# Performance work log

Hardware: AMD Instinct MI355X
Metric: run time of the kernel (lower is better)

Reference implementation:

```python
import jax, jax.numpy as jnp
import numpy as np

E, H, V, P, RAW = 512, 1024, 12000, 36, 2048
B, L = 128, 21

def setup_inputs() -> dict:
    key = jax.random.key(0)
    ks = jax.random.split(key, 16)
    n = lambda k, sh: (0.02 * jax.random.normal(k, sh)).astype(jnp.float32)
    z = lambda sh: jnp.zeros(sh, jnp.float32)
    return {
        "images_features": jax.random.normal(ks[0], (B, P, RAW), dtype=jnp.float32),
        "encoded_captions": jax.random.randint(ks[1], (B, L), 0, V),
        "caption_lengths": L,
        "W_img": n(ks[2], (RAW, H)), "b_img": z((H,)),
        "W_glob": n(ks[3], (H, E)), "b_glob": z((E,)),
        "W_ih1": n(ks[4], (2 * E + H, 4 * H)), "W_hh1": n(ks[5], (H, 4 * H)),
        "b_ih1": z((4 * H,)), "b_hh1": z((4 * H,)),
        "Wx_gate": n(ks[6], (2 * E + H, H)), "bx_gate": z((H,)),
        "Wh_gate": n(ks[7], (H, H)), "bh_gate": z((H,)),
        "W_ih2": n(ks[8], (2 * H, 4 * H)), "W_hh2": n(ks[9], (H, 4 * H)),
        "b_ih2": z((4 * H,)), "b_hh2": z((4 * H,)),
        "Wv": n(ks[10], (H, P)), "bv": z((P,)),
        "Ws": n(ks[11], (H, P)), "bs": z((P,)),
        "Wg": n(ks[12], (H, P)),
        "wh": n(ks[13], (P,)),
        "emb": n(ks[14], (V, E)),
        "W_fc": n(ks[15], (H, V)), "b_fc": z((V,)),
    }

def _lstm(x, h, c, W_ih, W_hh, b_ih, b_hh):
    # torch LSTMCell gate order: i, f, g, o
    g = x @ W_ih + b_ih + h @ W_hh + b_hh
    i, f, gg, o = jnp.split(g, 4, axis=-1)
    c_new = jax.nn.sigmoid(f) * c + jax.nn.sigmoid(i) * jnp.tanh(gg)
    h_new = jax.nn.sigmoid(o) * jnp.tanh(c_new)
    return h_new, c_new

def reference(images_features, encoded_captions, caption_lengths, W_img, b_img,
              W_glob, b_glob, W_ih1, W_hh1, b_ih1, b_hh1, Wx_gate, bx_gate,
              Wh_gate, bh_gate, W_ih2, W_hh2, b_ih2, b_hh2, Wv, bv, Ws, bs,
              Wg, wh, emb, W_fc, b_fc):
    Bsz = images_features.shape[0]
    Hd = W_hh1.shape[0]
    T = int(caption_lengths) - 1
    Vfeat = jax.nn.relu(images_features @ W_img + b_img)            # (B,P,H)
    glob = jax.nn.relu(jnp.mean(Vfeat, axis=1) @ W_glob + b_glob)   # (B,E)
    img_proj = Vfeat @ Wv + bv                                      # (B,P,P) loop-invariant
    word_embs = emb[encoded_captions[:, :T]]                        # (B,T,E)

    def step(carry, we):
        h1, c1, h2, c2 = carry
        xt = jnp.concatenate([h2, glob, we], axis=-1)               # (B, H+2E)
        h1n, c1n = _lstm(xt, h1, c1, W_ih1, W_hh1, b_ih1, b_hh1)
        sen_gate = jax.nn.sigmoid(xt @ Wx_gate + bx_gate + h1 @ Wh_gate + bh_gate)
        st = sen_gate * jnp.tanh(c1n)                               # visual sentinel
        ht_proj = h1n @ Wg                                          # (B,P)
        z = jnp.tanh(img_proj + ht_proj[:, :, None]) @ wh           # (B,P)
        alpha = jax.nn.softmax(z, axis=1)                           # (B,P)
        context = jnp.einsum('bp,bph->bh', alpha, Vfeat)            # (B,H)
        att_vs = jnp.tanh(st @ Ws + bs + ht_proj) @ wh              # (B,)
        alpha_hat = jax.nn.softmax(jnp.concatenate([z, att_vs[:, None]], axis=1), axis=1)
        beta = alpha_hat[:, -1:]                                    # (B,1)
        c_hat = beta * st + (1.0 - beta) * context
        h2n, c2n = _lstm(jnp.concatenate([c_hat, h1n], axis=-1), h2, c2,
                         W_ih2, W_hh2, b_ih2, b_hh2)
        score = (c_hat + h2n) @ W_fc + b_fc                         # (B,V)
        return (h1n, c1n, h2n, c2n), (score, alpha, beta)

    zeros = jnp.zeros((Bsz, Hd), images_features.dtype)
    init = (zeros, zeros, zeros, zeros)
    _, (preds, alphas, betas) = jax.lax.scan(step, init, jnp.swapaxes(word_embs, 0, 1))
    return (jnp.swapaxes(preds, 0, 1),   # (B,T,V)
            jnp.swapaxes(alphas, 0, 1),  # (B,T,P)
            jnp.swapaxes(betas, 0, 1))   # (B,T,1)
```

## Files before the change

### kernel.cpp

```cpp
#include <hip/hip_runtime.h>
#include <hip/hip_bf16.h>
#include <math.h>

typedef __attribute__((ext_vector_type(4))) float f32x4;
typedef __attribute__((ext_vector_type(8))) short bf16x8;

constexpr int kB = 128, kT = 20, kH = 1024, kE = 512, kP = 36, kRaw = 2048, kV = 12000;
constexpr int kSlab1 = kB * 5120;
constexpr int kSlab2 = kB * 4096;

__device__ __forceinline__ float sigf(float x) { return 1.0f / (1.0f + expf(-x)); }

#define AS1C const __attribute__((address_space(1))) void*
#define AS3P __attribute__((address_space(3))) void*

constexpr int NZ1 = 2 * kB * kH / 4;
constexpr int NZ2 = 2 * kB * kH * 2 / 16;
constexpr int NCV = kB * kP * kRaw / 4;
constexpr int NPV = 64 * 1024 * 2 / 16;
constexpr int NPF = 32 * 1024 * 2 / 16;
constexpr int NPB = 5120;
constexpr int NGE = kB * kT * kE;

__global__ __launch_bounds__(256) void prep_small(
    float* c1z, uint4* h1z, const float* images, __hip_bfloat16* imagesb,
    uint4* wtv, uint4* wtfc_pad,
    const float* b_ih1, const float* b_hh1, const float* bx, const float* bh,
    const float* b_ih2, const float* b_hh2, float* bias_g1, float* bias_g2,
    const int* caps, const float* emb, __hip_bfloat16* wembb) {
  long idx = (long)blockIdx.x * 256 + threadIdx.x;
  if (idx < NZ1) { reinterpret_cast<float4*>(c1z)[idx] = make_float4(0, 0, 0, 0); return; }
  idx -= NZ1;
  if (idx < NZ2) { h1z[idx] = make_uint4(0, 0, 0, 0); return; }
  idx -= NZ2;
  if (idx < NCV) {
    float4 v = reinterpret_cast<const float4*>(images)[idx];
    __hip_bfloat16* d = imagesb + idx * 4;
    d[0] = __float2bfloat16(v.x); d[1] = __float2bfloat16(v.y);
    d[2] = __float2bfloat16(v.z); d[3] = __float2bfloat16(v.w);
    return;
  }
  idx -= NCV;
  if (idx < NPV) { wtv[idx] = make_uint4(0, 0, 0, 0); return; }
  idx -= NPV;
  if (idx < NPF) { wtfc_pad[idx] = make_uint4(0, 0, 0, 0); return; }
  idx -= NPF;
  if (idx < NPB) {
    int i = (int)idx;
    if (i < 4096) {
      bias_g1[i] = b_ih1[i] + b_hh1[i];
      bias_g2[i] = b_ih2[i] + b_hh2[i];
    } else {
      bias_g1[i] = bx[i - 4096] + bh[i - 4096];
    }
    return;
  }
  idx -= NPB;
  if (idx < NGE) {
    int e = (int)(idx % kE);
    int bt = (int)(idx / kE);
    int t = bt % kT;
    int b = bt / kT;
    int tok = caps[b * (kT + 1) + t];
    wembb[idx] = __float2bfloat16(emb[(size_t)tok * kE + e]);
  }
}

struct TJob {
  const float* src; __hip_bfloat16* dst;
  int ld_src, K, N, lddst, koff, noff, blk_off, nbx;
};
struct TAll { TJob job[12]; int njobs; int total_blocks; };

__global__ __launch_bounds__(256) void transpose_all(TAll ta) {
  __shared__ float t[32][33];
  int bid = blockIdx.x;
  int ji = 0;
  while (ji + 1 < ta.njobs && bid >= ta.job[ji + 1].blk_off) ++ji;
  const TJob& J = ta.job[ji];
  int lbid = bid - J.blk_off;
  int n0 = (lbid % J.nbx) * 32, k0 = (lbid / J.nbx) * 32;
  int tx = threadIdx.x & 31, ty = threadIdx.x >> 5;
  #pragma unroll
  for (int i = 0; i < 32; i += 8) {
    int k = k0 + ty + i, n = n0 + tx;
    t[ty + i][tx] = (k < J.K && n < J.N) ? J.src[(size_t)k * J.ld_src + n] : 0.0f;
  }
  __syncthreads();
  #pragma unroll
  for (int i = 0; i < 32; i += 8) {
    int n = n0 + ty + i, k = k0 + tx;
    if (n < J.N && k < J.K)
      J.dst[(size_t)(n + J.noff) * J.lddst + k + J.koff] = __float2bfloat16(t[tx][ty + i]);
  }
}

struct SegB { const __hip_bfloat16* A; int lda; int kstart; int kend; };
struct GemmBArgs {
  SegB seg[4]; int nseg;
  const __hip_bfloat16* WT; int ldk;
  const float* bias;
  float* C; __hip_bfloat16* C16; int ldc; int N; int Ktot; int act; int zstride;
};

__global__ __launch_bounds__(256) void gemm_bf16(GemmBArgs ga) {
  __shared__ char lds[65536];
  const int bm = blockIdx.y * 64;
  const int bn = blockIdx.x * 64;
  const int tid = threadIdx.x;
  const int lane = tid & 63;
  const int w = tid >> 6;
  const int wr = w >> 1, wc = w & 1;

  int rowS[4], scbS[4], dstS[4];
  #pragma unroll
  for (int j = 0; j < 4; ++j) {
    int off = ((j * 4 + w) * 64 + lane) * 16;
    int row = off >> 8, colb = off & 255;
    rowS[j] = row;
    scbS[j] = colb ^ ((row & 7) << 4);
    dstS[j] = (j * 4 + w) * 1024;
  }

  f32x4 acc[2][2] = {};
  const int nz = gridDim.z;
  const int nit = (ga.Ktot >> 7) / nz;
  const int it0 = blockIdx.z * nit;
  float* C = ga.C + (size_t)blockIdx.z * ga.zstride;

  auto stage = [&](int it, int buf) {
    const int k0 = it << 7;
    int si = 0;
    while (k0 >= ga.seg[si].kend) ++si;
    const __hip_bfloat16* Aseg = ga.seg[si].A;
    const int lda = ga.seg[si].lda;
    const int ks = k0 - ga.seg[si].kstart;
    char* baseA = lds + buf * 32768;
    char* baseB = baseA + 16384;
    #pragma unroll
    for (int j = 0; j < 4; ++j) {
      const __hip_bfloat16* sA = Aseg + (size_t)(bm + rowS[j]) * lda + ks + (scbS[j] >> 1);
      __builtin_amdgcn_global_load_lds((AS1C)sA, (AS3P)(baseA + dstS[j]), 16, 0, 0);
      const __hip_bfloat16* sB = ga.WT + (size_t)(bn + rowS[j]) * ga.ldk + k0 + (scbS[j] >> 1);
      __builtin_amdgcn_global_load_lds((AS1C)sB, (AS3P)(baseB + dstS[j]), 16, 0, 0);
    }
  };

  auto compute = [&](int buf) {
    const char* baseA = lds + buf * 32768;
    const char* baseB = baseA + 16384;
    #pragma unroll
    for (int kk = 0; kk < 4; ++kk) {
      bf16x8 a[2], b[2];
      #pragma unroll
      for (int f = 0; f < 2; ++f) {
        int row = wr * 32 + f * 16 + (lane & 15);
        int cb = kk * 64 + (lane >> 4) * 16;
        a[f] = *(const bf16x8*)(baseA + row * 256 + (cb ^ ((row & 7) << 4)));
        int nl = wc * 32 + f * 16 + (lane & 15);
        b[f] = *(const bf16x8*)(baseB + nl * 256 + (cb ^ ((nl & 7) << 4)));
      }
      #pragma unroll
      for (int fm = 0; fm < 2; ++fm)
        #pragma unroll
        for (int fn = 0; fn < 2; ++fn)
          acc[fm][fn] = __builtin_amdgcn_mfma_f32_16x16x32_bf16(a[fm], b[fn], acc[fm][fn], 0, 0, 0);
    }
  };

  stage(it0, 0);
  stage(it0 + 1, 1);
  asm volatile("s_waitcnt vmcnt(8)" ::: "memory");
  __builtin_amdgcn_s_barrier();
  int cur = 0;
  for (int i = 0; i < nit; ++i) {
    compute(cur);
    __builtin_amdgcn_s_barrier();
    if (i + 2 < nit) stage(it0 + i + 2, cur);
    if (i + 1 < nit) {
      if (i + 2 < nit) asm volatile("s_waitcnt vmcnt(8)" ::: "memory");
      else             asm volatile("s_waitcnt vmcnt(0)" ::: "memory");
      __builtin_amdgcn_s_barrier();
    }
    cur ^= 1;
  }

  #pragma unroll
  for (int fm = 0; fm < 2; ++fm) {
    int rbase = bm + wr * 32 + fm * 16 + (lane >> 4) * 4;
    #pragma unroll
    for (int fn = 0; fn < 2; ++fn) {
      int col = bn + wc * 32 + fn * 16 + (lane & 15);
      if (col >= ga.N) continue;
      float bv = ga.bias ? ga.bias[col] : 0.0f;
      #pragma unroll
      for (int j = 0; j < 4; ++j) {
        float v = acc[fm][fn][j] + bv;
        if (ga.act == 1) v = fmaxf(v, 0.0f);
        size_t off = (size_t)(rbase + j) * ga.ldc + col;
        if (ga.C) C[off] = v;
        if (ga.C16) ga.C16[off] = __float2bfloat16(v);
      }
    }
  }
}

struct G128Args {
  const __hip_bfloat16* A; int lda;
  const __hip_bfloat16* WT; int ldk;
  const float* bias;
  float* C; __hip_bfloat16* C16; int ldc; int N; int Ktot; int act; int cmap; int morder;
};

template <int BK>
__global__ __launch_bounds__(256) void gemm128(G128Args ga) {
  constexpr int RB = BK * 2;
  constexpr int TILEB = 128 * RB;
  constexpr int ROUNDS = TILEB / 4096;
  constexpr int SWZ = (RB == 256) ? 15 : (RB == 128 ? 7 : 3);
  __shared__ char lds[2 * 2 * TILEB];
  const int gx = gridDim.x;
  const int gy = gridDim.y;
  const int nwg = gx * gy;
  int bid = blockIdx.y * gx + blockIdx.x;
  int q = nwg >> 3, r = nwg & 7;
  int xc = bid & 7, yq = bid >> 3;
  int swz = (xc < r ? xc * (q + 1) : r * (q + 1) + (xc - r) * q) + yq;
  int bn, bm;
  if (ga.morder == 1) { bm = (swz % gy) * 128; bn = (swz / gy) * 128; }
  else                { bn = (swz % gx) * 128; bm = (swz / gx) * 128; }

  const int tid = threadIdx.x;
  const int lane = tid & 63;
  const int w = tid >> 6;
  const int wr = w >> 1, wc = w & 1;

  int rowS[ROUNDS], scbS[ROUNDS], dstS[ROUNDS];
  #pragma unroll
  for (int j = 0; j < ROUNDS; ++j) {
    int off = ((j * 4 + w) * 64 + lane) * 16;
    int row = off / RB, colb = off % RB;
    rowS[j] = row;
    scbS[j] = colb ^ ((row & SWZ) << 4);
    dstS[j] = off;
  }

  f32x4 acc[4][4] = {};
  const int nit = ga.Ktot / BK;

  auto stage = [&](int it, int buf) {
    const int k0 = it * BK;
    char* baseA = lds + buf * 2 * TILEB;
    char* baseB = baseA + TILEB;
    #pragma unroll
    for (int j = 0; j < ROUNDS; ++j) {
      const __hip_bfloat16* sA = ga.A + (size_t)(bm + rowS[j]) * ga.lda + k0 + (scbS[j] >> 1);
      __builtin_amdgcn_global_load_lds((AS1C)sA, (AS3P)(baseA + dstS[j]), 16, 0, 0);
      const __hip_bfloat16* sB = ga.WT + (size_t)(bn + rowS[j]) * ga.ldk + k0 + (scbS[j] >> 1);
      __builtin_amdgcn_global_load_lds((AS1C)sB, (AS3P)(baseB + dstS[j]), 16, 0, 0);
    }
  };

  auto compute = [&](int buf) {
    const char* baseA = lds + buf * 2 * TILEB;
    const char* baseB = baseA + TILEB;
    #pragma unroll
    for (int kk = 0; kk < BK / 32; ++kk) {
      bf16x8 a[4], b[4];
      int cb = kk * 64 + (lane >> 4) * 16;
      #pragma unroll
      for (int f = 0; f < 4; ++f) {
        int row = wr * 64 + f * 16 + (lane & 15);
        a[f] = *(const bf16x8*)(baseA + row * RB + (cb ^ ((row & SWZ) << 4)));
        int nl = wc * 64 + f * 16 + (lane & 15);
        b[f] = *(const bf16x8*)(baseB + nl * RB + (cb ^ ((nl & SWZ) << 4)));
      }
      #pragma unroll
      for (int fm = 0; fm < 4; ++fm)
        #pragma unroll
        for (int fn = 0; fn < 4; ++fn)
          acc[fm][fn] = __builtin_amdgcn_mfma_f32_16x16x32_bf16(a[fm], b[fn], acc[fm][fn], 0, 0, 0);
    }
  };

  auto wait_one_stage = [&]() {
    if constexpr (ROUNDS == 4) asm volatile("s_waitcnt vmcnt(8)" ::: "memory");
    else                       asm volatile("s_waitcnt vmcnt(4)" ::: "memory");
  };

  stage(0, 0);
  stage(1, 1);
  wait_one_stage();
  __builtin_amdgcn_s_barrier();
  int cur = 0;
  for (int i = 0; i < nit; ++i) {
    compute(cur);
    __builtin_amdgcn_s_barrier();
    if (i + 2 < nit) stage(i + 2, cur);
    if (i + 1 < nit) {
      if (i + 2 < nit) wait_one_stage();
      else             asm volatile("s_waitcnt vmcnt(0)" ::: "memory");
      __builtin_amdgcn_s_barrier();
    }
    cur ^= 1;
  }

  #pragma unroll
  for (int fm = 0; fm < 4; ++fm) {
    int rbase = bm + wr * 64 + fm * 16 + (lane >> 4) * 4;
    #pragma unroll
    for (int fn = 0; fn < 4; ++fn) {
      int col = bn + wc * 64 + fn * 16 + (lane & 15);
      if (col >= ga.N) continue;
      float bv = ga.bias ? ga.bias[col] : 0.0f;
      #pragma unroll
      for (int j = 0; j < 4; ++j) {
        float v = acc[fm][fn][j] + bv;
        if (ga.act == 1) v = fmaxf(v, 0.0f);
        int m = rbase + j;
        size_t off = ga.cmap == 1
            ? (size_t)(m & 127) * ga.ldc + (size_t)(m >> 7) * kV + col
            : (size_t)m * ga.ldc + col;
        if (ga.C) ga.C[off] = v;
        if (ga.C16) ga.C16[off] = __float2bfloat16(v);
      }
    }
  }
}

__global__ __launch_bounds__(256) void mean_p(const float* __restrict__ Vfeat,
                                              __hip_bfloat16* __restrict__ meanVb) {
  int idx = blockIdx.x * 256 + threadIdx.x;
  if (idx >= kB * kH) return;
  int b = idx >> 10, h = idx & 1023;
  float sm = 0.0f;
  for (int p = 0; p < kP; ++p) sm += Vfeat[((size_t)b * kP + p) * kH + h];
  meanVb[idx] = __float2bfloat16(sm * (1.0f / kP));
}

__global__ __launch_bounds__(256) void step1_fused(
    const float* __restrict__ g, const float* __restrict__ bias_g1,
    float* __restrict__ c1, __hip_bfloat16* __restrict__ h1b,
    const float* __restrict__ img_proj, const float* __restrict__ Vfeat,
    const float* __restrict__ Wg, const float* __restrict__ Ws,
    const float* __restrict__ bs, const float* __restrict__ wh,
    float* __restrict__ c_hat, __hip_bfloat16* __restrict__ c_hatb,
    float* __restrict__ out_alphas, float* __restrict__ out_betas, int t) {
  const int b = blockIdx.x;
  const int tid = threadIdx.x;
  const int lane = tid & 63;
  const int w = tid >> 6;
  __shared__ float sh_h1[kH];
  __shared__ float sh_st[kH];
  __shared__ float wsum[4][36];
  __shared__ float htp[36];
  __shared__ float stp[36];
  __shared__ float alpha[kP];
  __shared__ float sred[4];

  const float* gr0 = g + (size_t)b * 5120;
  const float* gr1 = gr0 + kSlab1;
  const float* gr2 = gr1 + kSlab1;
  #pragma unroll
  for (int i = 0; i < 4; ++i) {
    int h = tid + i * 256;
    float ig = sigf(gr0[h]           + gr1[h]           + gr2[h]           + bias_g1[h]);
    float fg = sigf(gr0[kH + h]      + gr1[kH + h]      + gr2[kH + h]      + bias_g1[kH + h]);
    float gg = tanhf(gr0[2 * kH + h] + gr1[2 * kH + h]  + gr2[2 * kH + h]  + bias_g1[2 * kH + h]);
    float og = sigf(gr0[3 * kH + h]  + gr1[3 * kH + h]  + gr2[3 * kH + h]  + bias_g1[3 * kH + h]);
    int idx = b * kH + h;
    float c = fg * c1[idx] + ig * gg;
    float tc = tanhf(c);
    float hn = og * tc;
    c1[idx] = c;
    h1b[idx] = __float2bfloat16(hn);
    sh_h1[h] = hn;
    sh_st[h] = sigf(gr0[4 * kH + h] + gr1[4 * kH + h] + gr2[4 * kH + h] + bias_g1[4 * kH + h]) * tc;
  }
  __syncthreads();

  #pragma unroll
  for (int pass = 0; pass < 2; ++pass) {
    const float* vec = pass == 0 ? sh_h1 : sh_st;
    const float* W = pass == 0 ? Wg : Ws;
    float pg[36];
    #pragma unroll
    for (int j = 0; j < 36; ++j) pg[j] = 0.0f;
    #pragma unroll
    for (int i = 0; i < 4; ++i) {
      int hh = tid + i * 256;
      float hv = vec[hh];
      const float4* wrow = reinterpret_cast<const float4*>(W + (size_t)hh * 36);
      #pragma unroll
      for (int r = 0; r < 9; ++r) {
        float4 wv = wrow[r];
        pg[4 * r + 0] = fmaf(hv, wv.x, pg[4 * r + 0]);
        pg[4 * r + 1] = fmaf(hv, wv.y, pg[4 * r + 1]);
        pg[4 * r + 2] = fmaf(hv, wv.z, pg[4 * r + 2]);
        pg[4 * r + 3] = fmaf(hv, wv.w, pg[4 * r + 3]);
      }
    }
    #pragma unroll
    for (int j = 0; j < 36; ++j) {
      float v = pg[j];
      #pragma unroll
      for (int off = 32; off > 0; off >>= 1) v += __shfl_down(v, off, 64);
      if (lane == 0) wsum[w][j] = v;
    }
    __syncthreads();
    if (tid < 36) {
      float s = wsum[0][tid] + wsum[1][tid] + wsum[2][tid] + wsum[3][tid];
      if (pass == 0) htp[tid] = s; else stp[tid] = s;
    }
    __syncthreads();
  }

  if (w == 0) {
    float zz_r = -3.0e38f;
    if (lane < kP) {
      const float* ip = img_proj + ((size_t)b * kP + lane) * kP;
      float acc = 0.0f;
      #pragma unroll
      for (int j = 0; j < kP; ++j) acc = fmaf(tanhf(ip[j] + htp[j]), wh[j], acc);
      zz_r = acc;
    }
    float m = zz_r;
    #pragma unroll
    for (int off = 32; off > 0; off >>= 1) m = fmaxf(m, __shfl_xor(m, off, 64));
    float e = (lane < kP) ? expf(zz_r - m) : 0.0f;
    float s = e;
    #pragma unroll
    for (int off = 32; off > 0; off >>= 1) s += __shfl_xor(s, off, 64);
    if (lane < kP) alpha[lane] = e / s;
    if (lane == 0) { sred[2] = m; sred[3] = s; }
  } else if (w == 1) {
    float tv = 0.0f;
    if (lane < kP) tv = tanhf(stp[lane] + bs[lane] + htp[lane]) * wh[lane];
    #pragma unroll
    for (int off = 32; off > 0; off >>= 1) tv += __shfl_xor(tv, off, 64);
    if (lane == 0) sred[0] = tv;
  }
  __syncthreads();
  if (tid == 0) {
    float av = sred[0], m = sred[2], s = sred[3];
    float m2 = fmaxf(m, av);
    float eb = expf(av - m2);
    float beta = eb / (s * expf(m - m2) + eb);
    sred[1] = beta;
    out_betas[b * kT + t] = beta;
  }
  __syncthreads();
  if (tid < kP) out_alphas[((size_t)b * kT + t) * kP + tid] = alpha[tid];
  const float beta = sred[1];
  #pragma unroll
  for (int i = 0; i < 4; ++i) {
    int h = tid + i * 256;
    float ctx = 0.0f;
    for (int p = 0; p < kP; ++p) ctx = fmaf(alpha[p], Vfeat[((size_t)b * kP + p) * kH + h], ctx);
    float v = beta * sh_st[h] + (1.0f - beta) * ctx;
    c_hat[(size_t)b * kH + h] = v;
    c_hatb[(size_t)b * kH + h] = __float2bfloat16(v);
  }
}

__global__ __launch_bounds__(256) void lstm2_elem(const float* __restrict__ g,
                                                  const float* __restrict__ bias_g2,
                                                  float* __restrict__ c2,
                                                  __hip_bfloat16* __restrict__ h2b,
                                                  const float* __restrict__ c_hat,
                                                  __hip_bfloat16* __restrict__ sbufb) {
  int idx = blockIdx.x * 256 + threadIdx.x;
  if (idx >= kB * kH) return;
  int b = idx >> 10, h = idx & 1023;
  const float* gr0 = g + (size_t)b * 4 * kH;
  const float* gr1 = gr0 + kSlab2;
  const float* gr2 = gr1 + kSlab2;
  float ig = sigf(gr0[h]           + gr1[h]           + gr2[h]           + bias_g2[h]);
  float fg = sigf(gr0[kH + h]      + gr1[kH + h]      + gr2[kH + h]      + bias_g2[kH + h]);
  float gg = tanhf(gr0[2 * kH + h] + gr1[2 * kH + h]  + gr2[2 * kH + h]  + bias_g2[2 * kH + h]);
  float og = sigf(gr0[3 * kH + h]  + gr1[3 * kH + h]  + gr2[3 * kH + h]  + bias_g2[3 * kH + h]);
  float c = fg * c2[idx] + ig * gg;
  float hn = og * tanhf(c);
  c2[idx] = c;
  h2b[idx] = __float2bfloat16(hn);
  sbufb[idx] = __float2bfloat16(c_hat[idx] + hn);
}

extern "C" void kernel_launch(void* const* d_in, const int* in_sizes, int n_in,
                              void* d_out, int out_size, void* d_ws, size_t ws_size,
                              hipStream_t stream) {
  const float* images  = (const float*)d_in[0];
  const int*   caps    = (const int*)d_in[1];
  const float* W_img   = (const float*)d_in[3];
  const float* b_img   = (const float*)d_in[4];
  const float* W_glob  = (const float*)d_in[5];
  const float* b_glob  = (const float*)d_in[6];
  const float* W_ih1   = (const float*)d_in[7];
  const float* W_hh1   = (const float*)d_in[8];
  const float* b_ih1   = (const float*)d_in[9];
  const float* b_hh1   = (const float*)d_in[10];
  const float* Wx_gate = (const float*)d_in[11];
  const float* bx_gate = (const float*)d_in[12];
  const float* Wh_gate = (const float*)d_in[13];
  const float* bh_gate = (const float*)d_in[14];
  const float* W_ih2   = (const float*)d_in[15];
  const float* W_hh2   = (const float*)d_in[16];
  const float* b_ih2   = (const float*)d_in[17];
  const float* b_hh2   = (const float*)d_in[18];
  const float* Wv      = (const float*)d_in[19];
  const float* bv      = (const float*)d_in[20];
  const float* Ws_     = (const float*)d_in[21];
  const float* bs_     = (const float*)d_in[22];
  const float* Wg      = (const float*)d_in[23];
  const float* wh      = (const float*)d_in[24];
  const float* emb     = (const float*)d_in[25];
  const float* W_fc    = (const float*)d_in[26];
  const float* b_fc    = (const float*)d_in[27];

  float* out = (float*)d_out;
  float* out_alphas = out + (size_t)kB * kT * kV;
  float* out_betas  = out_alphas + (size_t)kB * kT * kP;

  char* base = (char*)d_ws;
  auto alloc = [&](size_t bytes) {
    char* p = base;
    base += (bytes + 255) & ~(size_t)255;
    return p;
  };
  float*          Vfeat   = (float*)alloc((size_t)kB * kP * kH * 4);
  __hip_bfloat16* Vfeatb  = (__hip_bfloat16*)alloc((size_t)kB * kP * kH * 2);
  __hip_bfloat16* imagesb = (__hip_bfloat16*)alloc((size_t)kB * kP * kRaw * 2);
  __hip_bfloat16* WTg1    = (__hip_bfloat16*)alloc((size_t)5120 * 3072 * 2);
  __hip_bfloat16* WTg2    = (__hip_bfloat16*)alloc((size_t)4096 * 3072 * 2);
  __hip_bfloat16* WTfc    = (__hip_bfloat16*)alloc((size_t)12032 * 1024 * 2);
  __hip_bfloat16* WTimg   = (__hip_bfloat16*)alloc((size_t)1024 * 2048 * 2);
  __hip_bfloat16* WTglob  = (__hip_bfloat16*)alloc((size_t)512 * 1024 * 2);
  __hip_bfloat16* WTv     = (__hip_bfloat16*)alloc((size_t)64 * 1024 * 2);
  __hip_bfloat16* wembb   = (__hip_bfloat16*)alloc((size_t)kB * kT * kE * 2);
  float*          img_proj= (float*)alloc((size_t)kB * kP * kP * 4);
  __hip_bfloat16* globb   = (__hip_bfloat16*)alloc((size_t)kB * kE * 2);
  __hip_bfloat16* meanVb  = (__hip_bfloat16*)alloc((size_t)kB * kH * 2);
  float*          c1      = (float*)alloc((size_t)2 * kB * kH * 4);
  float*          c2      = c1 + kB * kH;
  __hip_bfloat16* h1b     = (__hip_bfloat16*)alloc((size_t)2 * kB * kH * 2);
  __hip_bfloat16* h2b     = h1b + kB * kH;
  float*          g1out   = (float*)alloc((size_t)3 * kB * 5120 * 4);
  float*          chat    = (float*)alloc((size_t)kB * kH * 4);
  __hip_bfloat16* chatb   = (__hip_bfloat16*)alloc((size_t)kB * kH * 2);
  __hip_bfloat16* sbufall = (__hip_bfloat16*)alloc((size_t)kT * kB * kH * 2);
  float*          bias_g1 = (float*)alloc(5120 * 4);
  float*          bias_g2 = (float*)alloc(4096 * 4);

  {
    long total = (long)NZ1 + NZ2 + NCV + NPV + NPF + NPB + NGE;
    int blocks = (int)((total + 255) / 256);
    prep_small<<<blocks, 256, 0, stream>>>(
        c1, (uint4*)h1b, images, imagesb, (uint4*)WTv,
        (uint4*)(WTfc + (size_t)12000 * 1024),
        b_ih1, b_hh1, bx_gate, bh_gate, b_ih2, b_hh2, bias_g1, bias_g2,
        caps, emb, wembb);
  }
  {
    TAll ta = {};
    int off = 0, j = 0;
    auto add = [&](const float* src, int ldsrc, int K, int N, __hip_bfloat16* dst,
                   int lddst, int koff, int noff) {
      int nbx = (N + 31) / 32, nby = (K + 31) / 32;
      ta.job[j] = {src, dst, ldsrc, K, N, lddst, koff, noff, off, nbx};
      off += nbx * nby;
      ++j;
    };
    add(W_img,   kH,     kRaw, kH,     WTimg,  kRaw, 0, 0);
    add(W_glob,  kE,     kH,   kE,     WTglob, kH,   0, 0);
    add(Wv,      kP,     kH,   kP,     WTv,    kH,   0, 0);
    add(W_ih1,   4 * kH, 2048, 4 * kH, WTg1,   3072, 0, 0);
    add(W_hh1,   4 * kH, 1024, 4 * kH, WTg1,   3072, 2048, 0);
    add(Wx_gate, kH,     2048, kH,     WTg1,   3072, 0, 4096);
    add(Wh_gate, kH,     1024, kH,     WTg1,   3072, 2048, 4096);
    add(W_ih2,   4 * kH, 2048, 4 * kH, WTg2,   3072, 0, 0);
    add(W_hh2,   4 * kH, 1024, 4 * kH, WTg2,   3072, 2048, 0);
    add(W_fc,    kV,     kH,   kV,     WTfc,   kH,   0, 0);
    ta.njobs = j;
    ta.total_blocks = off;
    transpose_all<<<off, 256, 0, stream>>>(ta);
  }

  {
    G128Args ga = {};
    ga.A = imagesb; ga.lda = kRaw; ga.WT = WTimg; ga.ldk = kRaw; ga.bias = b_img;
    ga.C = Vfeat; ga.C16 = Vfeatb; ga.ldc = kH; ga.N = kH; ga.Ktot = kRaw;
    ga.act = 1; ga.cmap = 0; ga.morder = 0;
    gemm128<64><<<dim3(kH / 128, kB * kP / 128), 256, 0, stream>>>(ga);
  }
  mean_p<<<(kB * kH + 255) / 256, 256, 0, stream>>>(Vfeat, meanVb);
  {
    GemmBArgs ga = {};
    ga.seg[0] = {meanVb, kH, 0, kH};
    ga.nseg = 1; ga.WT = WTglob; ga.ldk = kH; ga.bias = b_glob;
    ga.C = nullptr; ga.C16 = globb; ga.ldc = kE; ga.N = kE; ga.Ktot = kH; ga.act = 1;
    gemm_bf16<<<dim3(kE / 64, kB / 64, 1), 256, 0, stream>>>(ga);
  }
  {
    GemmBArgs ga = {};
    ga.seg[0] = {Vfeatb, kH, 0, kH};
    ga.nseg = 1; ga.WT = WTv; ga.ldk = kH; ga.bias = bv;
    ga.C = img_proj; ga.C16 = nullptr; ga.ldc = kP; ga.N = kP; ga.Ktot = kH; ga.act = 0;
    gemm_bf16<<<dim3(1, kB * kP / 64, 1), 256, 0, stream>>>(ga);
  }

  for (int t = 0; t < kT; ++t) {
    {
      GemmBArgs ga = {};
      ga.seg[0] = {h2b, kH, 0, kH};
      ga.seg[1] = {globb, kE, kH, kH + kE};
      ga.seg[2] = {wembb + (size_t)t * kE, kT * kE, kH + kE, 2048};
      ga.seg[3] = {h1b, kH, 2048, 3072};
      ga.nseg = 4; ga.WT = WTg1; ga.ldk = 3072; ga.bias = nullptr;
      ga.C = g1out; ga.C16 = nullptr; ga.ldc = 5120; ga.N = 5120; ga.Ktot = 3072;
      ga.act = 0; ga.zstride = kSlab1;
      gemm_bf16<<<dim3(5120 / 64, kB / 64, 3), 256, 0, stream>>>(ga);
    }
    step1_fused<<<kB, 256, 0, stream>>>(g1out, bias_g1, c1, h1b, img_proj, Vfeat,
                                        Wg, Ws_, bs_, wh, chat, chatb,
                                        out_alphas, out_betas, t);
    {
      GemmBArgs ga = {};
      ga.seg[0] = {chatb, kH, 0, kH};
      ga.seg[1] = {h1b, kH, kH, 2048};
      ga.seg[2] = {h2b, kH, 2048, 3072};
      ga.nseg = 3; ga.WT = WTg2; ga.ldk = 3072; ga.bias = nullptr;
      ga.C = g1out; ga.C16 = nullptr; ga.ldc = 4096; ga.N = 4096; ga.Ktot = 3072;
      ga.act = 0; ga.zstride = kSlab2;
      gemm_bf16<<<dim3(4096 / 64, kB / 64, 3), 256, 0, stream>>>(ga);
    }
    lstm2_elem<<<(kB * kH + 255) / 256, 256, 0, stream>>>(
        g1out, bias_g2, c2, h2b, chat, sbufall + (size_t)t * kB * kH);
  }

  {
    G128Args ga = {};
    ga.A = sbufall; ga.lda = kH; ga.WT = WTfc; ga.ldk = kH; ga.bias = b_fc;
    ga.C = out; ga.C16 = nullptr; ga.ldc = kT * kV; ga.N = kV; ga.Ktot = kH;
    ga.act = 0; ga.cmap = 1; ga.morder = 1;
    gemm128<32><<<dim3(12032 / 128, kT * kB / 128), 256, 0, stream>>>(ga);
  }
}
```

Baseline: 1.537 ms.

## Raise split-K to four slabs, add nontemporal output stores, fix LDS dest offset

Split-K in both per-step LSTM gate GEMMs goes from 3 to 4 z-slices, with the elementwise kernels summing four partial slabs. This adds blocks to the small M=128 recurrent GEMMs for better CU occupancy, at the cost of an extra partial buffer to write and read. The final vocab-projection GEMM now writes its large fp32 output with nontemporal stores to reduce cache pollution. The LDS destination offset in gemm128 is also changed to a per-wave base, as global_load_lds expects.

```diff
diff --git a/kernel.cpp b/kernel.cpp
--- a/kernel.cpp
+++ b/kernel.cpp
@@ -209,7 +209,8 @@
   const __hip_bfloat16* A; int lda;
   const __hip_bfloat16* WT; int ldk;
   const float* bias;
-  float* C; __hip_bfloat16* C16; int ldc; int N; int Ktot; int act; int cmap; int morder;
+  float* C; __hip_bfloat16* C16; int ldc; int N; int Ktot; int act; int cmap;
+  int morder; int nt;
 };
 
 template <int BK>
@@ -242,7 +243,7 @@
     int row = off / RB, colb = off % RB;
     rowS[j] = row;
     scbS[j] = colb ^ ((row & SWZ) << 4);
-    dstS[j] = off;
+    dstS[j] = (j * 4 + w) * 1024;
   }
 
   f32x4 acc[4][4] = {};
@@ -321,7 +322,10 @@
         size_t off = ga.cmap == 1
             ? (size_t)(m & 127) * ga.ldc + (size_t)(m >> 7) * kV + col
             : (size_t)m * ga.ldc + col;
-        if (ga.C) ga.C[off] = v;
+        if (ga.C) {
+          if (ga.nt) __builtin_nontemporal_store(v, &ga.C[off]);
+          else       ga.C[off] = v;
+        }
         if (ga.C16) ga.C16[off] = __float2bfloat16(v);
       }
     }
@@ -361,21 +365,23 @@
   const float* gr0 = g + (size_t)b * 5120;
   const float* gr1 = gr0 + kSlab1;
   const float* gr2 = gr1 + kSlab1;
+  const float* gr3 = gr2 + kSlab1;
   #pragma unroll
   for (int i = 0; i < 4; ++i) {
     int h = tid + i * 256;
-    float ig = sigf(gr0[h]           + gr1[h]           + gr2[h]           + bias_g1[h]);
-    float fg = sigf(gr0[kH + h]      + gr1[kH + h]      + gr2[kH + h]      + bias_g1[kH + h]);
-    float gg = tanhf(gr0[2 * kH + h] + gr1[2 * kH + h]  + gr2[2 * kH + h]  + bias_g1[2 * kH + h]);
-    float og = sigf(gr0[3 * kH + h]  + gr1[3 * kH + h]  + gr2[3 * kH + h]  + bias_g1[3 * kH + h]);
+    float pi = gr0[h] + gr1[h] + gr2[h] + gr3[h] + bias_g1[h];
+    float pf = gr0[kH + h] + gr1[kH + h] + gr2[kH + h] + gr3[kH + h] + bias_g1[kH + h];
+    float pg = gr0[2 * kH + h] + gr1[2 * kH + h] + gr2[2 * kH + h] + gr3[2 * kH + h] + bias_g1[2 * kH + h];
+    float po = gr0[3 * kH + h] + gr1[3 * kH + h] + gr2[3 * kH + h] + gr3[3 * kH + h] + bias_g1[3 * kH + h];
+    float ps = gr0[4 * kH + h] + gr1[4 * kH + h] + gr2[4 * kH + h] + gr3[4 * kH + h] + bias_g1[4 * kH + h];
     int idx = b * kH + h;
-    float c = fg * c1[idx] + ig * gg;
+    float c = sigf(pf) * c1[idx] + sigf(pi) * tanhf(pg);
     float tc = tanhf(c);
-    float hn = og * tc;
+    float hn = sigf(po) * tc;
     c1[idx] = c;
     h1b[idx] = __float2bfloat16(hn);
     sh_h1[h] = hn;
-    sh_st[h] = sigf(gr0[4 * kH + h] + gr1[4 * kH + h] + gr2[4 * kH + h] + bias_g1[4 * kH + h]) * tc;
+    sh_st[h] = sigf(ps) * tc;
   }
   __syncthreads();
 
@@ -475,12 +481,13 @@
   const float* gr0 = g + (size_t)b * 4 * kH;
   const float* gr1 = gr0 + kSlab2;
   const float* gr2 = gr1 + kSlab2;
-  float ig = sigf(gr0[h]           + gr1[h]           + gr2[h]           + bias_g2[h]);
-  float fg = sigf(gr0[kH + h]      + gr1[kH + h]      + gr2[kH + h]      + bias_g2[kH + h]);
-  float gg = tanhf(gr0[2 * kH + h] + gr1[2 * kH + h]  + gr2[2 * kH + h]  + bias_g2[2 * kH + h]);
-  float og = sigf(gr0[3 * kH + h]  + gr1[3 * kH + h]  + gr2[3 * kH + h]  + bias_g2[3 * kH + h]);
-  float c = fg * c2[idx] + ig * gg;
-  float hn = og * tanhf(c);
+  const float* gr3 = gr2 + kSlab2;
+  float pi = gr0[h] + gr1[h] + gr2[h] + gr3[h] + bias_g2[h];
+  float pf = gr0[kH + h] + gr1[kH + h] + gr2[kH + h] + gr3[kH + h] + bias_g2[kH + h];
+  float pg = gr0[2 * kH + h] + gr1[2 * kH + h] + gr2[2 * kH + h] + gr3[2 * kH + h] + bias_g2[2 * kH + h];
+  float po = gr0[3 * kH + h] + gr1[3 * kH + h] + gr2[3 * kH + h] + gr3[3 * kH + h] + bias_g2[3 * kH + h];
+  float c = sigf(pf) * c2[idx] + sigf(pi) * tanhf(pg);
+  float hn = sigf(po) * tanhf(c);
   c2[idx] = c;
   h2b[idx] = __float2bfloat16(hn);
   sbufb[idx] = __float2bfloat16(c_hat[idx] + hn);
@@ -544,7 +551,7 @@
   float*          c2      = c1 + kB * kH;
   __hip_bfloat16* h1b     = (__hip_bfloat16*)alloc((size_t)2 * kB * kH * 2);
   __hip_bfloat16* h2b     = h1b + kB * kH;
-  float*          g1out   = (float*)alloc((size_t)3 * kB * 5120 * 4);
+  float*          g1out   = (float*)alloc((size_t)4 * kB * 5120 * 4);
   float*          chat    = (float*)alloc((size_t)kB * kH * 4);
   __hip_bfloat16* chatb   = (__hip_bfloat16*)alloc((size_t)kB * kH * 2);
   __hip_bfloat16* sbufall = (__hip_bfloat16*)alloc((size_t)kT * kB * kH * 2);
@@ -589,7 +596,7 @@
     G128Args ga = {};
     ga.A = imagesb; ga.lda = kRaw; ga.WT = WTimg; ga.ldk = kRaw; ga.bias = b_img;
     ga.C = Vfeat; ga.C16 = Vfeatb; ga.ldc = kH; ga.N = kH; ga.Ktot = kRaw;
-    ga.act = 1; ga.cmap = 0; ga.morder = 0;
+    ga.act = 1; ga.cmap = 0; ga.morder = 0; ga.nt = 0;
     gemm128<64><<<dim3(kH / 128, kB * kP / 128), 256, 0, stream>>>(ga);
   }
   mean_p<<<(kB * kH + 255) / 256, 256, 0, stream>>>(Vfeat, meanVb);
@@ -618,7 +625,7 @@
       ga.nseg = 4; ga.WT = WTg1; ga.ldk = 3072; ga.bias = nullptr;
       ga.C = g1out; ga.C16 = nullptr; ga.ldc = 5120; ga.N = 5120; ga.Ktot = 3072;
       ga.act = 0; ga.zstride = kSlab1;
-      gemm_bf16<<<dim3(5120 / 64, kB / 64, 3), 256, 0, stream>>>(ga);
+      gemm_bf16<<<dim3(5120 / 64, kB / 64, 4), 256, 0, stream>>>(ga);
     }
     step1_fused<<<kB, 256, 0, stream>>>(g1out, bias_g1, c1, h1b, img_proj, Vfeat,
                                         Wg, Ws_, bs_, wh, chat, chatb,
@@ -631,7 +638,7 @@
       ga.nseg = 3; ga.WT = WTg2; ga.ldk = 3072; ga.bias = nullptr;
       ga.C = g1out; ga.C16 = nullptr; ga.ldc = 4096; ga.N = 4096; ga.Ktot = 3072;
       ga.act = 0; ga.zstride = kSlab2;
-      gemm_bf16<<<dim3(4096 / 64, kB / 64, 3), 256, 0, stream>>>(ga);
+      gemm_bf16<<<dim3(4096 / 64, kB / 64, 4), 256, 0, stream>>>(ga);
     }
     lstm2_elem<<<(kB * kH + 255) / 256, 256, 0, stream>>>(
         g1out, bias_g2, c2, h2b, chat, sbufall + (size_t)t * kB * kH);
@@ -641,7 +648,7 @@
     G128Args ga = {};
     ga.A = sbufall; ga.lda = kH; ga.WT = WTfc; ga.ldk = kH; ga.bias = b_fc;
     ga.C = out; ga.C16 = nullptr; ga.ldc = kT * kV; ga.N = kV; ga.Ktot = kH;
-    ga.act = 0; ga.cmap = 1; ga.morder = 1;
+    ga.act = 0; ga.cmap = 1; ga.morder = 1; ga.nt = 1;
     gemm128<32><<<dim3(12032 / 128, kT * kB / 128), 256, 0, stream>>>(ga);
   }
 }
```

Result: no change. 1.567 ms (+1.9%).
